# Kernel tuning notes

Hardware: AMD Instinct MI355X
Metric: run time of the kernel (lower is better)

Reference implementation:

```python
import jax, jax.numpy as jnp
import numpy as np

B, S = 128, 512
VOCAB, E, H, T = 100000, 100, 128, 10  # tagset_size=10 -> CRF over T-1=9 tags
HD = H // 2  # per-direction LSTM hidden


def setup_inputs():
    key = jax.random.key(0)
    ks = jax.random.split(key, 14)
    s = 0.08
    inputs = jax.random.randint(ks[0], (B, S), 1, VOCAB)
    tags = jax.random.randint(ks[1], (B, S), 1, T)  # valid after tags-1 shift
    mask = jnp.ones((B, S), dtype=bool)
    emb = (jax.random.normal(ks[2], (VOCAB, E)) * s).at[0].set(0.0)  # padding_idx=0 row zeroed
    Wih_f = jax.random.normal(ks[3], (4 * HD, E)) * s
    Whh_f = jax.random.normal(ks[4], (4 * HD, HD)) * s
    b_f = jax.random.normal(ks[5], (4 * HD,)) * s
    Wih_b = jax.random.normal(ks[6], (4 * HD, E)) * s
    Whh_b = jax.random.normal(ks[7], (4 * HD, HD)) * s
    b_b = jax.random.normal(ks[8], (4 * HD,)) * s
    W_out = jax.random.normal(ks[9], (T, H)) * s
    b_out = jax.random.normal(ks[10], (T,)) * s
    start = jax.random.normal(ks[11], (T - 1,)) * s
    end = jax.random.normal(ks[12], (T - 1,)) * s
    trans = jax.random.normal(ks[13], (T - 1, T - 1)) * s
    return dict(inputs=inputs, tags=tags, mask=mask, emb=emb,
                Wih_f=Wih_f, Whh_f=Whh_f, b_f=b_f,
                Wih_b=Wih_b, Whh_b=Whh_b, b_b=b_b,
                W_out=W_out, b_out=b_out, start=start, end=end, trans=trans)


def _lstm_dir(x, Wih, Whh, b, reverse):
    # x: [S, B, E] time-major; PyTorch gate order i,f,g,o; b = b_ih + b_hh
    h0 = jnp.zeros((x.shape[1], Whh.shape[1]), x.dtype)

    def step(carry, xt):
        h, c = carry
        gates = xt @ Wih.T + h @ Whh.T + b
        i, f, g, o = jnp.split(gates, 4, axis=-1)
        c = jax.nn.sigmoid(f) * c + jax.nn.sigmoid(i) * jnp.tanh(g)
        h = jax.nn.sigmoid(o) * jnp.tanh(c)
        return (h, c), h

    _, hs = jax.lax.scan(step, (h0, h0), x, reverse=reverse)
    return hs  # [S, B, HD]


def _crf_nll(em, tags, mask, start, end, trans):
    # Linear-chain CRF (torchcrf-style). em: [S,B,K], tags/mask: [S,B]
    pick = lambda e, t: jnp.take_along_axis(e, t[:, None], axis=-1)[:, 0]
    # numerator: score of the gold path
    score0 = start[tags[0]] + pick(em[0], tags[0])

    def num_step(sc, inp):
        em_t, t, tp, m = inp
        return sc + jnp.where(m, trans[tp, t] + pick(em_t, t), 0.0), None

    score, _ = jax.lax.scan(num_step, score0, (em[1:], tags[1:], tags[:-1], mask[1:]))
    last_idx = mask.sum(0).astype(jnp.int32) - 1
    last_tags = jnp.take_along_axis(tags, last_idx[None, :], axis=0)[0]
    score = score + end[last_tags]
    # denominator: forward algorithm (log partition)
    alpha0 = start[None, :] + em[0]  # [B,K]

    def fwd_step(alpha, inp):
        em_t, m = inp
        nxt = jax.nn.logsumexp(alpha[:, :, None] + trans[None, :, :] + em_t[:, None, :], axis=1)
        return jnp.where(m[:, None], nxt, alpha), None

    alpha, _ = jax.lax.scan(fwd_step, alpha0, (em[1:], mask[1:]))
    logZ = jax.nn.logsumexp(alpha + end[None, :], axis=1)
    return -(score - logZ).mean()  # loss = -log_likelihood.mean()


def _forward(inputs, tags, mask, emb, Wih_f, Whh_f, b_f, Wih_b, Whh_b, b_b, W_out, b_out, start, end, trans):
    x = emb[inputs].transpose(1, 0, 2)  # [S,B,E]
    h = jnp.concatenate([_lstm_dir(x, Wih_f, Whh_f, b_f, False),
                         _lstm_dir(x, Wih_b, Whh_b, b_b, True)], axis=-1)  # [S,B,H]
    # dropout is identity at eval; slice off tag 0 as in the module
    em = (h @ W_out.T + b_out)[:, :, 1:]  # [S,B,T-1]
    return _crf_nll(em, (tags - 1).T, mask.T, start, end, trans)


def reference(inputs, tags, mask, emb, Wih_f, Whh_f, b_f, Wih_b, Whh_b, b_b, W_out, b_out, start, end, trans):
    return _forward(inputs, tags, mask, emb, Wih_f, Whh_f, b_f, Wih_b, Whh_b, b_b, W_out, b_out, start, end, trans)
```

## Files before the change

kernel.cpp:

```cpp
#include <hip/hip_runtime.h>
#include <math.h>

#define SB 512
#define NB 128
#define HD 64

typedef _Float16 h2 __attribute__((ext_vector_type(2)));
typedef _Float16 f16x8 __attribute__((ext_vector_type(8)));
typedef float f32x4 __attribute__((ext_vector_type(4)));
union U4 { uint4 u; h2 h[4]; _Float16 f[8]; };
union UF { uint4 u; f16x8 h8; _Float16 f[8]; };
union U2 { uint2 u; _Float16 f[4]; };
union UH { unsigned u; _Float16 f[2]; };

__device__ __forceinline__ float frcp(float x) { return __builtin_amdgcn_rcpf(x); }
__device__ __forceinline__ float fsig(float x) { return frcp(1.0f + __expf(-x)); }
__device__ __forceinline__ float ftanh(float x) {
    float t = __expf(-2.0f * fabsf(x));
    float r = (1.0f - t) * frcp(1.0f + t);
    return copysignf(r, x);
}
__device__ __forceinline__ float fdot2(h2 a, h2 b, float c) {
    return __builtin_amdgcn_fdot2(a, b, c, false);
}

__global__ void prep_kernel(const float* __restrict__ Wih_f, const float* __restrict__ Wih_bb,
                            const float* __restrict__ Whh_f, const float* __restrict__ Whh_bb,
                            const float* __restrict__ b_f, const float* __restrict__ b_bb,
                            const float* __restrict__ trans,
                            unsigned* __restrict__ W2h, unsigned* __restrict__ whh16,
                            float* __restrict__ bias2, float* __restrict__ Eexp)
{
    int idx = blockIdx.x * 256 + threadIdx.x;
    if (idx < 32768) {
        int col = idx >> 6, d = idx & 63;
        int dir = col >> 8, r = col & 255, j = r >> 2, g = r & 3;
        const float* src = (dir ? Wih_bb : Wih_f) + (g * 64 + j) * 100;
        UH u; u.u = 0;
        if (d < 50) { u.f[0] = (_Float16)src[2 * d]; u.f[1] = (_Float16)src[2 * d + 1]; }
        W2h[idx] = u.u;
    } else if (idx < 49152) {
        int d = idx - 32768;
        int kp = d & 31, u = (d >> 5) & 63, g = (d >> 11) & 3, dir = d >> 13;
        const float* src = (dir ? Whh_bb : Whh_f) + (g * 64 + u) * 64 + 2 * kp;
        UH uu; uu.f[0] = (_Float16)src[0]; uu.f[1] = (_Float16)src[1];
        int k4 = kp >> 2, q = kp & 3;
        whh16[(((dir * 4 + g) * 8 + k4) * 64 + u) * 4 + q] = uu.u;
    } else if (idx < 49664) {
        int col = idx - 49152;
        int dir = col >> 8, r = col & 255, j = r >> 2, g = r & 3;
        bias2[col] = (dir ? b_bb : b_f)[g * 64 + j];
    } else if (idx < 49745) {
        int i = idx - 49664;
        Eexp[i] = __expf(trans[i]);
    }
}

__global__ __launch_bounds__(256, 2) void gemm_kernel(
    const int* __restrict__ inputs, const float* __restrict__ emb,
    const unsigned* __restrict__ W2h, const float* __restrict__ bias2,
    _Float16* __restrict__ xgh)
{
    __shared__ __align__(16) unsigned sE[128 * 68];
    __shared__ __align__(16) unsigned sW[128 * 68];
    __shared__ float sbias[512];
    __shared__ int stok[128];
    const int tt = blockIdx.x;
    const int tid = threadIdx.x;
    const int w = tid >> 6, l = tid & 63;
    const int q = l >> 4, n = l & 15;

    if (tid < 128) stok[tid] = inputs[tid * SB + tt];
    for (int i = tid; i < 512; i += 256) sbias[i] = bias2[i];
    __syncthreads();
    for (int idx = tid; idx < 8192; idx += 256) {
        int row = idx >> 6, d = idx & 63;
        unsigned v = 0;
        if (d < 50) {
            const float* ep = emb + (size_t)stok[row] * 100 + 2 * d;
            UH u; u.f[0] = (_Float16)ep[0]; u.f[1] = (_Float16)ep[1];
            v = u.u;
        }
        sE[row * 68 + d] = v;
    }

    for (int cg = 0; cg < 4; ++cg) {
        __syncthreads();
        for (int idx = tid; idx < 2048; idx += 256)
            ((uint4*)sW)[(idx >> 4) * 17 + (idx & 15)] = ((const uint4*)W2h)[cg * 2048 + idx];
        __syncthreads();

        f32x4 acc[2][8];
        #pragma unroll
        for (int m = 0; m < 2; ++m)
            #pragma unroll
            for (int c = 0; c < 8; ++c)
                #pragma unroll
                for (int r = 0; r < 4; ++r) acc[m][c][r] = 0.f;

        #pragma unroll
        for (int kt = 0; kt < 4; ++kt) {
            const int ko = 16 * kt + 2 * q;
            UF A0, A1;
            {
                const unsigned* rp = &sE[(16 * (2 * w + 0) + n) * 68 + ko];
                uint2 lo = *(const uint2*)rp;
                uint2 hi = *(const uint2*)(rp + 8);
                A0.u = make_uint4(lo.x, lo.y, hi.x, hi.y);
                rp = &sE[(16 * (2 * w + 1) + n) * 68 + ko];
                lo = *(const uint2*)rp;
                hi = *(const uint2*)(rp + 8);
                A1.u = make_uint4(lo.x, lo.y, hi.x, hi.y);
            }
            UF B[8];
            #pragma unroll
            for (int c = 0; c < 8; ++c) {
                const unsigned* rp = &sW[(16 * c + n) * 68 + ko];
                uint2 lo = *(const uint2*)rp;
                uint2 hi = *(const uint2*)(rp + 8);
                B[c].u = make_uint4(lo.x, lo.y, hi.x, hi.y);
            }
            #pragma unroll
            for (int c = 0; c < 8; ++c) {
                acc[0][c] = __builtin_amdgcn_mfma_f32_16x16x32_f16(A0.h8, B[c].h8, acc[0][c], 0, 0, 0);
                acc[1][c] = __builtin_amdgcn_mfma_f32_16x16x32_f16(A1.h8, B[c].h8, acc[1][c], 0, 0, 0);
            }
        }

        #pragma unroll
        for (int m = 0; m < 2; ++m)
            #pragma unroll
            for (int c = 0; c < 8; ++c) {
                int col = cg * 128 + 16 * c + n;
                float bc = sbias[col];
                #pragma unroll
                for (int r = 0; r < 4; ++r) {
                    int row = 16 * (2 * w + m) + 4 * q + r;
                    xgh[(size_t)(tt * NB + row) * 512 + col] = (_Float16)(acc[m][c][r] + bc);
                }
            }
    }
}

__global__ __attribute__((amdgpu_flat_work_group_size(64, 64), amdgpu_waves_per_eu(1, 1)))
void lstm_kernel(
    const _Float16* __restrict__ xgh, const unsigned* __restrict__ whh16,
    _Float16* __restrict__ h16)
{
    const int blk = blockIdx.x;
    const int b = blk & (NB - 1);
    const int dir = blk >> 7;
    const int j = threadIdx.x;

    __shared__ __align__(16) unsigned wlds[8192];
    __shared__ __align__(16) _Float16 hbuf[64];

    {
        const uint4* src = (const uint4*)(whh16 + dir * 8192);
        uint4* dst = (uint4*)wlds;
        #pragma unroll
        for (int i = 0; i < 32; ++i) dst[i * 64 + j] = src[i * 64 + j];
    }
    hbuf[j] = (_Float16)0.f;
    float c = 0.f;

    const int t0 = dir ? (SB - 1) : 0;
    const ptrdiff_t xstride = (dir ? -1 : 1) * (ptrdiff_t)(NB * 512);
    const _Float16* xp = xgh + ((size_t)(t0 * NB + b)) * 512 + dir * 256 + j * 4;
    _Float16* hp = h16 + ((size_t)(b * 2 + dir) * SB + t0) * 64 + j;
    const ptrdiff_t hstride = (dir ? -1 : 1) * (ptrdiff_t)64;

    U2 p0, p1, p2;
    p0.u = *(const uint2*)xp;
    p1.u = *(const uint2*)(xp + xstride);
    p2.u = *(const uint2*)(xp + 2 * xstride);
    const _Float16* xq = xp + 3 * xstride;

    const uint4* wl = (const uint4*)wlds;

    for (int s = 0; s < SB; ++s) {
        float a0 = (float)p0.f[0], a1 = (float)p0.f[1];
        float a2 = (float)p0.f[2], a3 = (float)p0.f[3];
        p0 = p1; p1 = p2;
        p2.u = *(const uint2*)xq;
        xq += xstride;

        U4 hv[8];
        #pragma unroll
        for (int k4 = 0; k4 < 8; ++k4) hv[k4].u = *(const uint4*)&hbuf[k4 * 8];

        float g0[4] = {a0, 0.f, 0.f, 0.f};
        float g1[4] = {a1, 0.f, 0.f, 0.f};
        float g2[4] = {a2, 0.f, 0.f, 0.f};
        float g3[4] = {a3, 0.f, 0.f, 0.f};
        #pragma unroll
        for (int k4 = 0; k4 < 8; ++k4) {
            U4 w0, w1, w2, w3;
            w0.u = wl[(0 * 8 + k4) * 64 + j];
            w1.u = wl[(1 * 8 + k4) * 64 + j];
            w2.u = wl[(2 * 8 + k4) * 64 + j];
            w3.u = wl[(3 * 8 + k4) * 64 + j];
            const int p = k4 & 3;
            #pragma unroll
            for (int q = 0; q < 4; ++q) {
                g0[p] = fdot2(hv[k4].h[q], w0.h[q], g0[p]);
                g1[p] = fdot2(hv[k4].h[q], w1.h[q], g1[p]);
                g2[p] = fdot2(hv[k4].h[q], w2.h[q], g2[p]);
                g3[p] = fdot2(hv[k4].h[q], w3.h[q], g3[p]);
            }
        }
        a0 = (g0[0] + g0[1]) + (g0[2] + g0[3]);
        a1 = (g1[0] + g1[1]) + (g1[2] + g1[3]);
        a2 = (g2[0] + g2[1]) + (g2[2] + g2[3]);
        a3 = (g3[0] + g3[1]) + (g3[2] + g3[3]);

        float ig = fsig(a0), fg = fsig(a1), gg = ftanh(a2), og = fsig(a3);
        c = fg * c + ig * gg;
        float h = og * ftanh(c);
        *hp = (_Float16)h;
        hp += hstride;
        hbuf[j] = (_Float16)h;
    }
}

__global__ __launch_bounds__(256, 1) void pgs_kernel(
    const _Float16* __restrict__ h16, const float* __restrict__ W_out,
    const float* __restrict__ b_out, const int* __restrict__ tags,
    const float* __restrict__ startv, const float* __restrict__ endv,
    const float* __restrict__ trans, const float* __restrict__ Eexp,
    float* __restrict__ em0, float* __restrict__ gold, float* __restrict__ Pws)
{
    __shared__ __align__(16) unsigned tile[128 * 64];
    __shared__ __align__(16) float em3L[SB * 12];
    __shared__ __align__(16) unsigned sWo[9 * 64];
    __shared__ float sb[9];
    const int b = blockIdx.x, tid = threadIdx.x;

    for (int i2 = tid; i2 < 576; i2 += 256) {
        int k = i2 >> 6, jp = i2 & 63;
        const float* src = W_out + (k + 1) * 128 + 2 * jp;
        UH u; u.f[0] = (_Float16)src[0]; u.f[1] = (_Float16)src[1];
        sWo[i2] = u.u;
    }
    if (tid < 9) sb[tid] = b_out[1 + tid];

    for (int tt = 0; tt < 4; ++tt) {
        const int t0 = tt * 128;
        __syncthreads();
        #pragma unroll
        for (int dir = 0; dir < 2; ++dir) {
            const unsigned* src = (const unsigned*)(h16 + ((size_t)(b * 2 + dir) * SB + t0) * 64);
            for (int i = tid; i < 4096; i += 256) {
                int t = i >> 5, jp = i & 31;
                tile[t * 64 + dir * 32 + jp] = src[i];
            }
        }
        __syncthreads();

        for (int o = tid; o < 1152; o += 256) {
            int tl = o / 9, k = o - 9 * tl;
            const U4* hr = (const U4*)&tile[tl * 64];
            const U4* wr = (const U4*)&sWo[k * 64];
            float pa = 0.f, pb = 0.f;
            #pragma unroll
            for (int qq = 0; qq < 16; qq += 2) {
                U4 hv = hr[qq], wv = wr[qq];
                U4 hv2 = hr[qq + 1], wv2 = wr[qq + 1];
                #pragma unroll
                for (int z = 0; z < 4; ++z) {
                    pa = fdot2(hv.h[z], wv.h[z], pa);
                    pb = fdot2(hv2.h[z], wv2.h[z], pb);
                }
            }
            em3L[(t0 + tl) * 12 + k] = pa + pb + sb[k];
        }
    }
    __syncthreads();

    if (tid >= 128 && tid < 137)
        em0[b * 12 + (tid - 128)] = em3L[tid - 128];

    if (tid >= 64 && tid < 128) {
        const int l = tid - 64;
        const int* tb = tags + (size_t)b * SB;
        float sc = 0.f;
        for (int t = l; t < SB; t += 64) {
            int tg = tb[t] - 1;
            if (t > 0) {
                int tp = tb[t - 1] - 1;
                sc += trans[tp * 9 + tg] + em3L[t * 12 + tg];
            }
        }
        if (l == 0) {
            int tg0 = tb[0] - 1, tgl = tb[SB - 1] - 1;
            sc += startv[tg0] + em3L[tg0] + endv[tgl];
        }
        #pragma unroll
        for (int off = 32; off > 0; off >>= 1) sc += __shfl_down(sc, off);
        if (l == 0) gold[b] = sc;
    }

    if (tid < 32) {
        const int c = tid;
        float E[81];
        #pragma unroll
        for (int i = 0; i < 81; ++i) E[i] = Eexp[i];

        float P[81];
        #pragma unroll
        for (int i = 0; i < 81; ++i) P[i] = 0.f;
        #pragma unroll
        for (int i = 0; i < 9; ++i) P[i * 9 + i] = 1.f;
        float M = 0.f;

        const int t0 = 1 + 16 * c;
        const int nst = (t0 + 16 <= SB) ? 16 : (SB - t0);
        const float* ep = &em3L[t0 * 12];

        for (int s = 0; s < nst; ++s, ep += 12) {
            float4 e0 = *(const float4*)ep;
            float4 e1 = *(const float4*)(ep + 4);
            float e8 = ep[8];
            float ex[9] = { __expf(e0.x), __expf(e0.y), __expf(e0.z), __expf(e0.w),
                            __expf(e1.x), __expf(e1.y), __expf(e1.z), __expf(e1.w),
                            __expf(e8) };
            #pragma unroll
            for (int i = 0; i < 9; ++i) {
                float tmp[9];
                #pragma unroll
                for (int jj = 0; jj < 9; ++jj) tmp[jj] = P[i * 9] * E[jj];
                #pragma unroll
                for (int k = 1; k < 9; ++k)
                    #pragma unroll
                    for (int jj = 0; jj < 9; ++jj) tmp[jj] += P[i * 9 + k] * E[k * 9 + jj];
                #pragma unroll
                for (int jj = 0; jj < 9; ++jj) P[i * 9 + jj] = tmp[jj] * ex[jj];
            }
            if ((s & 3) == 3) {
                float mx = P[0];
                #pragma unroll
                for (int i = 1; i < 81; ++i) mx = fmaxf(mx, P[i]);
                M += __logf(mx);
                float r = frcp(mx);
                #pragma unroll
                for (int i = 0; i < 81; ++i) P[i] *= r;
            }
        }

        float* dst = Pws + ((size_t)b * 32 + c) * 84;
        #pragma unroll
        for (int i = 0; i < 81; ++i) dst[i] = P[i];
        dst[81] = M;
    }
}

__global__ __launch_bounds__(128, 1) void crf_combine(
    const float* __restrict__ em0, const float* __restrict__ Pws,
    const float* __restrict__ gold, const float* __restrict__ startv,
    const float* __restrict__ endv, float* __restrict__ out)
{
    const int b = threadIdx.x;
    float A[9], M = 0.f;
    {
        const float* eb = em0 + (size_t)b * 12;
        float4 e0 = *(const float4*)eb;
        float4 e1 = *(const float4*)(eb + 4);
        float e[9] = { e0.x, e0.y, e0.z, e0.w, e1.x, e1.y, e1.z, e1.w, eb[8] };
        #pragma unroll
        for (int k = 0; k < 9; ++k) A[k] = __expf(startv[k] + e[k]);
    }

    for (int c = 0; c < 32; ++c) {
        const float4* src = (const float4*)(Pws + ((size_t)b * 32 + c) * 84);
        float buf[84];
        #pragma unroll
        for (int qq = 0; qq < 21; ++qq) {
            float4 v = src[qq];
            buf[4 * qq] = v.x; buf[4 * qq + 1] = v.y; buf[4 * qq + 2] = v.z; buf[4 * qq + 3] = v.w;
        }
        float tmp[9];
        #pragma unroll
        for (int jj = 0; jj < 9; ++jj) tmp[jj] = A[0] * buf[jj];
        #pragma unroll
        for (int i = 1; i < 9; ++i)
            #pragma unroll
            for (int jj = 0; jj < 9; ++jj) tmp[jj] += A[i] * buf[i * 9 + jj];
        float mx = tmp[0];
        #pragma unroll
        for (int jj = 1; jj < 9; ++jj) mx = fmaxf(mx, tmp[jj]);
        M += __logf(mx) + buf[81];
        float r = frcp(mx);
        #pragma unroll
        for (int jj = 0; jj < 9; ++jj) A[jj] = tmp[jj] * r;
    }

    float Z = 0.f;
    #pragma unroll
    for (int k = 0; k < 9; ++k) Z += A[k] * __expf(endv[k]);
    float part = M + __logf(Z) - gold[b];

    #pragma unroll
    for (int off = 32; off > 0; off >>= 1) part += __shfl_down(part, off);
    __shared__ float sm[2];
    if ((b & 63) == 0) sm[b >> 6] = part;
    __syncthreads();
    if (b == 0) out[0] = (sm[0] + sm[1]) * (1.0f / NB);
}

extern "C" void kernel_launch(void* const* d_in, const int* in_sizes, int n_in,
                              void* d_out, int out_size, void* d_ws, size_t ws_size,
                              hipStream_t stream)
{
    const int*   inputs = (const int*)d_in[0];
    const int*   tags   = (const int*)d_in[1];
    const float* emb    = (const float*)d_in[3];
    const float* Wih_f  = (const float*)d_in[4];
    const float* Whh_f  = (const float*)d_in[5];
    const float* b_f    = (const float*)d_in[6];
    const float* Wih_b  = (const float*)d_in[7];
    const float* Whh_b  = (const float*)d_in[8];
    const float* b_b    = (const float*)d_in[9];
    const float* W_out  = (const float*)d_in[10];
    const float* b_out  = (const float*)d_in[11];
    const float* startv = (const float*)d_in[12];
    const float* endv   = (const float*)d_in[13];
    const float* transv = (const float*)d_in[14];

    char* w = (char*)d_ws;
    float* em0     = (float*)w;     w += (size_t)NB * SB * 12 * 4;
    _Float16* xgh  = (_Float16*)w;  w += (size_t)SB * NB * 512 * 2;
    _Float16* h16  = (_Float16*)w;  w += (size_t)NB * 2 * SB * 64 * 2;
    float* Pws     = (float*)w;     w += (size_t)NB * 32 * 84 * 4;
    float* gold    = (float*)w;     w += NB * 4;
    unsigned* W2h  = (unsigned*)w;  w += 32768 * 4;
    unsigned* whh16= (unsigned*)w;  w += 16384 * 4;
    float* bias2   = (float*)w;     w += 512 * 4;
    float* Eexp    = (float*)w;     w += 81 * 4;

    prep_kernel<<<195, 256, 0, stream>>>(Wih_f, Wih_b, Whh_f, Whh_b, b_f, b_b, transv,
                                         W2h, whh16, bias2, Eexp);
    gemm_kernel<<<SB, 256, 0, stream>>>(inputs, emb, W2h, bias2, xgh);
    lstm_kernel<<<256, 64, 0, stream>>>(xgh, whh16, h16);
    pgs_kernel<<<NB, 256, 0, stream>>>(h16, W_out, b_out, tags, startv, endv, transv,
                                       Eexp, em0, gold, Pws);
    crf_combine<<<1, 128, 0, stream>>>(em0, Pws, gold, startv, endv, (float*)d_out);
}
```

Before: 487.1 us.

## Fold weight prep into consumers and fuse CRF combine into per-batch kernel

Removes the separate prep kernel. The GEMM and LSTM kernels now convert fp32 weights to fp16 while loading them into shared memory, and pgs computes exp(trans) in shared memory. The per-batch 32-chunk CRF combine moves into pgs_kernel through shared memory, leaving a tiny final reduction kernel. This cuts a launch and global round-trips for Pws, em0 and gold, at the cost of redundant weight conversion in every GEMM and LSTM block. The combine loop now runs on 64 threads that all do the same work.

```diff
diff --git a/kernel.cpp b/kernel.cpp
--- a/kernel.cpp
+++ b/kernel.cpp
@@ -24,41 +24,10 @@
     return __builtin_amdgcn_fdot2(a, b, c, false);
 }
 
-__global__ void prep_kernel(const float* __restrict__ Wih_f, const float* __restrict__ Wih_bb,
-                            const float* __restrict__ Whh_f, const float* __restrict__ Whh_bb,
-                            const float* __restrict__ b_f, const float* __restrict__ b_bb,
-                            const float* __restrict__ trans,
-                            unsigned* __restrict__ W2h, unsigned* __restrict__ whh16,
-                            float* __restrict__ bias2, float* __restrict__ Eexp)
-{
-    int idx = blockIdx.x * 256 + threadIdx.x;
-    if (idx < 32768) {
-        int col = idx >> 6, d = idx & 63;
-        int dir = col >> 8, r = col & 255, j = r >> 2, g = r & 3;
-        const float* src = (dir ? Wih_bb : Wih_f) + (g * 64 + j) * 100;
-        UH u; u.u = 0;
-        if (d < 50) { u.f[0] = (_Float16)src[2 * d]; u.f[1] = (_Float16)src[2 * d + 1]; }
-        W2h[idx] = u.u;
-    } else if (idx < 49152) {
-        int d = idx - 32768;
-        int kp = d & 31, u = (d >> 5) & 63, g = (d >> 11) & 3, dir = d >> 13;
-        const float* src = (dir ? Whh_bb : Whh_f) + (g * 64 + u) * 64 + 2 * kp;
-        UH uu; uu.f[0] = (_Float16)src[0]; uu.f[1] = (_Float16)src[1];
-        int k4 = kp >> 2, q = kp & 3;
-        whh16[(((dir * 4 + g) * 8 + k4) * 64 + u) * 4 + q] = uu.u;
-    } else if (idx < 49664) {
-        int col = idx - 49152;
-        int dir = col >> 8, r = col & 255, j = r >> 2, g = r & 3;
-        bias2[col] = (dir ? b_bb : b_f)[g * 64 + j];
-    } else if (idx < 49745) {
-        int i = idx - 49664;
-        Eexp[i] = __expf(trans[i]);
-    }
-}
-
 __global__ __launch_bounds__(256, 2) void gemm_kernel(
     const int* __restrict__ inputs, const float* __restrict__ emb,
-    const unsigned* __restrict__ W2h, const float* __restrict__ bias2,
+    const float* __restrict__ Wih_f, const float* __restrict__ Wih_bb,
+    const float* __restrict__ b_f, const float* __restrict__ b_bb,
     _Float16* __restrict__ xgh)
 {
     __shared__ __align__(16) unsigned sE[128 * 68];
@@ -71,7 +40,10 @@
     const int q = l >> 4, n = l & 15;
 
     if (tid < 128) stok[tid] = inputs[tid * SB + tt];
-    for (int i = tid; i < 512; i += 256) sbias[i] = bias2[i];
+    for (int i = tid; i < 512; i += 256) {
+        int dir = i >> 8, r = i & 255, jj = r >> 2, g = r & 3;
+        sbias[i] = (dir ? b_bb : b_f)[g * 64 + jj];
+    }
     __syncthreads();
     for (int idx = tid; idx < 8192; idx += 256) {
         int row = idx >> 6, d = idx & 63;
@@ -86,8 +58,26 @@
 
     for (int cg = 0; cg < 4; ++cg) {
         __syncthreads();
-        for (int idx = tid; idx < 2048; idx += 256)
-            ((uint4*)sW)[(idx >> 4) * 17 + (idx & 15)] = ((const uint4*)W2h)[cg * 2048 + idx];
+        for (int idx = tid; idx < 2048; idx += 256) {
+            int col = cg * 128 + (idx >> 4);
+            int dir = col >> 8, r = col & 255, jj = r >> 2, g = r & 3;
+            const float* base = (dir ? Wih_bb : Wih_f) + (g * 64 + jj) * 100;
+            int dq = idx & 15;
+            UF pack; pack.u = make_uint4(0, 0, 0, 0);
+            if (dq < 12) {
+                float4 f0 = *(const float4*)(base + 8 * dq);
+                float4 f1 = *(const float4*)(base + 8 * dq + 4);
+                pack.f[0] = (_Float16)f0.x; pack.f[1] = (_Float16)f0.y;
+                pack.f[2] = (_Float16)f0.z; pack.f[3] = (_Float16)f0.w;
+                pack.f[4] = (_Float16)f1.x; pack.f[5] = (_Float16)f1.y;
+                pack.f[6] = (_Float16)f1.z; pack.f[7] = (_Float16)f1.w;
+            } else if (dq == 12) {
+                float4 f0 = *(const float4*)(base + 96);
+                pack.f[0] = (_Float16)f0.x; pack.f[1] = (_Float16)f0.y;
+                pack.f[2] = (_Float16)f0.z; pack.f[3] = (_Float16)f0.w;
+            }
+            ((uint4*)sW)[(idx >> 4) * 17 + dq] = pack.u;
+        }
         __syncthreads();
 
         f32x4 acc[2][8];
@@ -144,8 +134,8 @@
 
 __global__ __attribute__((amdgpu_flat_work_group_size(64, 64), amdgpu_waves_per_eu(1, 1)))
 void lstm_kernel(
-    const _Float16* __restrict__ xgh, const unsigned* __restrict__ whh16,
-    _Float16* __restrict__ h16)
+    const _Float16* __restrict__ xgh, const float* __restrict__ Whh_f,
+    const float* __restrict__ Whh_bb, _Float16* __restrict__ h16)
 {
     const int blk = blockIdx.x;
     const int b = blk & (NB - 1);
@@ -156,10 +146,21 @@
     __shared__ __align__(16) _Float16 hbuf[64];
 
     {
-        const uint4* src = (const uint4*)(whh16 + dir * 8192);
+        const float* Wsrc = dir ? Whh_bb : Whh_f;
         uint4* dst = (uint4*)wlds;
         #pragma unroll
-        for (int i = 0; i < 32; ++i) dst[i * 64 + j] = src[i * 64 + j];
+        for (int i = 0; i < 32; ++i) {
+            int g = i >> 3, k4 = i & 7;
+            const float* rp = Wsrc + (g * 64 + j) * 64 + 8 * k4;
+            float4 f0 = *(const float4*)rp;
+            float4 f1 = *(const float4*)(rp + 4);
+            UF pack;
+            pack.f[0] = (_Float16)f0.x; pack.f[1] = (_Float16)f0.y;
+            pack.f[2] = (_Float16)f0.z; pack.f[3] = (_Float16)f0.w;
+            pack.f[4] = (_Float16)f1.x; pack.f[5] = (_Float16)f1.y;
+            pack.f[6] = (_Float16)f1.z; pack.f[7] = (_Float16)f1.w;
+            dst[i * 64 + j] = pack.u;
+        }
     }
     hbuf[j] = (_Float16)0.f;
     float c = 0.f;
@@ -227,14 +228,16 @@
     const _Float16* __restrict__ h16, const float* __restrict__ W_out,
     const float* __restrict__ b_out, const int* __restrict__ tags,
     const float* __restrict__ startv, const float* __restrict__ endv,
-    const float* __restrict__ trans, const float* __restrict__ Eexp,
-    float* __restrict__ em0, float* __restrict__ gold, float* __restrict__ Pws)
+    const float* __restrict__ trans, float* __restrict__ parts)
 {
     __shared__ __align__(16) unsigned tile[128 * 64];
     __shared__ __align__(16) float em3L[SB * 12];
     __shared__ __align__(16) unsigned sWo[9 * 64];
     __shared__ float sb[9];
+    __shared__ float sEexp[81];
+    __shared__ float sgold;
     const int b = blockIdx.x, tid = threadIdx.x;
+    float* Pst = (float*)tile;
 
     for (int i2 = tid; i2 < 576; i2 += 256) {
         int k = i2 >> 6, jp = i2 & 63;
@@ -243,6 +246,7 @@
         sWo[i2] = u.u;
     }
     if (tid < 9) sb[tid] = b_out[1 + tid];
+    if (tid < 81) sEexp[tid] = __expf(trans[tid]);
 
     for (int tt = 0; tt < 4; ++tt) {
         const int t0 = tt * 128;
@@ -276,9 +280,6 @@
         }
     }
     __syncthreads();
-
-    if (tid >= 128 && tid < 137)
-        em0[b * 12 + (tid - 128)] = em3L[tid - 128];
 
     if (tid >= 64 && tid < 128) {
         const int l = tid - 64;
@@ -297,14 +298,14 @@
         }
         #pragma unroll
         for (int off = 32; off > 0; off >>= 1) sc += __shfl_down(sc, off);
-        if (l == 0) gold[b] = sc;
+        if (l == 0) sgold = sc;
     }
 
     if (tid < 32) {
         const int c = tid;
         float E[81];
         #pragma unroll
-        for (int i = 0; i < 81; ++i) E[i] = Eexp[i];
+        for (int i = 0; i < 81; ++i) E[i] = sEexp[i];
 
         float P[81];
         #pragma unroll
@@ -347,58 +348,55 @@
             }
         }
 
-        float* dst = Pws + ((size_t)b * 32 + c) * 84;
+        float* dst = &Pst[c * 84];
         #pragma unroll
         for (int i = 0; i < 81; ++i) dst[i] = P[i];
         dst[81] = M;
     }
-}
-
-__global__ __launch_bounds__(128, 1) void crf_combine(
-    const float* __restrict__ em0, const float* __restrict__ Pws,
-    const float* __restrict__ gold, const float* __restrict__ startv,
-    const float* __restrict__ endv, float* __restrict__ out)
+    __syncthreads();
+
+    if (tid < 64) {
+        float A[9], M = 0.f;
+        #pragma unroll
+        for (int k = 0; k < 9; ++k) A[k] = __expf(startv[k] + em3L[k]);
+
+        for (int c = 0; c < 32; ++c) {
+            const float4* src = (const float4*)&Pst[c * 84];
+            float buf[84];
+            #pragma unroll
+            for (int qq = 0; qq < 21; ++qq) {
+                float4 v = src[qq];
+                buf[4 * qq] = v.x; buf[4 * qq + 1] = v.y; buf[4 * qq + 2] = v.z; buf[4 * qq + 3] = v.w;
+            }
+            float tmp[9];
+            #pragma unroll
+            for (int jj = 0; jj < 9; ++jj) tmp[jj] = A[0] * buf[jj];
+            #pragma unroll
+            for (int i = 1; i < 9; ++i)
+                #pragma unroll
+                for (int jj = 0; jj < 9; ++jj) tmp[jj] += A[i] * buf[i * 9 + jj];
+            float mx = tmp[0];
+            #pragma unroll
+            for (int jj = 1; jj < 9; ++jj) mx = fmaxf(mx, tmp[jj]);
+            M += __logf(mx) + buf[81];
+            float r = frcp(mx);
+            #pragma unroll
+            for (int jj = 0; jj < 9; ++jj) A[jj] = tmp[jj] * r;
+        }
+
+        float Z = 0.f;
+        #pragma unroll
+        for (int k = 0; k < 9; ++k) Z += A[k] * __expf(endv[k]);
+        float part = M + __logf(Z) - sgold;
+        if (tid == 0) parts[b] = part;
+    }
+}
+
+__global__ __launch_bounds__(128, 1) void crf_combine2(
+    const float* __restrict__ parts, float* __restrict__ out)
 {
     const int b = threadIdx.x;
-    float A[9], M = 0.f;
-    {
-        const float* eb = em0 + (size_t)b * 12;
-        float4 e0 = *(const float4*)eb;
-        float4 e1 = *(const float4*)(eb + 4);
-        float e[9] = { e0.x, e0.y, e0.z, e0.w, e1.x, e1.y, e1.z, e1.w, eb[8] };
-        #pragma unroll
-        for (int k = 0; k < 9; ++k) A[k] = __expf(startv[k] + e[k]);
-    }
-
-    for (int c = 0; c < 32; ++c) {
-        const float4* src = (const float4*)(Pws + ((size_t)b * 32 + c) * 84);
-        float buf[84];
-        #pragma unroll
-        for (int qq = 0; qq < 21; ++qq) {
-            float4 v = src[qq];
-            buf[4 * qq] = v.x; buf[4 * qq + 1] = v.y; buf[4 * qq + 2] = v.z; buf[4 * qq + 3] = v.w;
-        }
-        float tmp[9];
-        #pragma unroll
-        for (int jj = 0; jj < 9; ++jj) tmp[jj] = A[0] * buf[jj];
-        #pragma unroll
-        for (int i = 1; i < 9; ++i)
-            #pragma unroll
-            for (int jj = 0; jj < 9; ++jj) tmp[jj] += A[i] * buf[i * 9 + jj];
-        float mx = tmp[0];
-        #pragma unroll
-        for (int jj = 1; jj < 9; ++jj) mx = fmaxf(mx, tmp[jj]);
-        M += __logf(mx) + buf[81];
-        float r = frcp(mx);
-        #pragma unroll
-        for (int jj = 0; jj < 9; ++jj) A[jj] = tmp[jj] * r;
-    }
-
-    float Z = 0.f;
-    #pragma unroll
-    for (int k = 0; k < 9; ++k) Z += A[k] * __expf(endv[k]);
-    float part = M + __logf(Z) - gold[b];
-
+    float part = parts[b];
     #pragma unroll
     for (int off = 32; off > 0; off >>= 1) part += __shfl_down(part, off);
     __shared__ float sm[2];
@@ -427,21 +425,13 @@
     const float* transv = (const float*)d_in[14];
 
     char* w = (char*)d_ws;
-    float* em0     = (float*)w;     w += (size_t)NB * SB * 12 * 4;
+    float* parts   = (float*)w;     w += (size_t)NB * SB * 12 * 4;
     _Float16* xgh  = (_Float16*)w;  w += (size_t)SB * NB * 512 * 2;
     _Float16* h16  = (_Float16*)w;  w += (size_t)NB * 2 * SB * 64 * 2;
-    float* Pws     = (float*)w;     w += (size_t)NB * 32 * 84 * 4;
-    float* gold    = (float*)w;     w += NB * 4;
-    unsigned* W2h  = (unsigned*)w;  w += 32768 * 4;
-    unsigned* whh16= (unsigned*)w;  w += 16384 * 4;
-    float* bias2   = (float*)w;     w += 512 * 4;
-    float* Eexp    = (float*)w;     w += 81 * 4;
-
-    prep_kernel<<<195, 256, 0, stream>>>(Wih_f, Wih_b, Whh_f, Whh_b, b_f, b_b, transv,
-                                         W2h, whh16, bias2, Eexp);
-    gemm_kernel<<<SB, 256, 0, stream>>>(inputs, emb, W2h, bias2, xgh);
-    lstm_kernel<<<256, 64, 0, stream>>>(xgh, whh16, h16);
-    pgs_kernel<<<NB, 256, 0, stream>>>(h16, W_out, b_out, tags, startv, endv, transv,
-                                       Eexp, em0, gold, Pws);
-    crf_combine<<<1, 128, 0, stream>>>(em0, Pws, gold, startv, endv, (float*)d_out);
-}
+    (void)w;
+
+    gemm_kernel<<<SB, 256, 0, stream>>>(inputs, emb, Wih_f, Wih_b, b_f, b_b, xgh);
+    lstm_kernel<<<256, 64, 0, stream>>>(xgh, Whh_f, Whh_b, h16);
+    pgs_kernel<<<NB, 256, 0, stream>>>(h16, W_out, b_out, tags, startv, endv, transv, parts);
+    crf_combine2<<<1, 128, 0, stream>>>(parts, (float*)d_out);
+}
```

Result: faster. 452.7 us (-7.1%).
